# Performance work log

Hardware: AMD Instinct MI355X
Metric: run time of the kernel (lower is better)

The kernel has to match this reference:

```python
import jax, jax.numpy as jnp
import numpy as np

N = 20000   # nodes
E = 100000  # edges per relation
R = 4       # relations
H = 4       # heads
D = 64      # embed_dim (per-head dim == embed_dim in this module)
F = 128     # node_feat_dim
L = 2       # layers
EPS = 1e-5  # torch LayerNorm default


def setup_inputs() -> dict:
    key = jax.random.key(0)
    ks = jax.random.split(key, 32)
    s = 0.05
    inp = {}
    inp["nodes"] = jnp.arange(N)
    inp["node_features"] = jax.random.normal(ks[0], (N, F), jnp.float32)
    inp["betweenness"] = jax.random.uniform(ks[1], (N,), jnp.float32)
    inp["closeness"] = jax.random.uniform(ks[2], (N,), jnp.float32)
    inp["node_sign_influence"] = jax.random.normal(ks[3], (N,), jnp.float32)
    inp["edge_src"] = jax.random.randint(ks[4], (R, E), 0, N)
    inp["edge_tgt"] = jax.random.randint(ks[5], (R, E), 0, N)
    # encoder params
    inp["enc_Wf"] = jax.random.normal(ks[6], (F, D), jnp.float32) * s
    inp["enc_bf"] = jnp.full((D,), 0.01, jnp.float32)
    inp["enc_Wc"] = jax.random.normal(ks[7], (2, D), jnp.float32) * s
    inp["enc_bc"] = jnp.full((D,), 0.01, jnp.float32)
    # per-layer, per-relation attention params
    inp["Wq"] = jax.random.normal(ks[8], (L, R, D, D * H), jnp.float32) * s
    inp["bq"] = jnp.zeros((L, R, D * H), jnp.float32)
    inp["Wk"] = jax.random.normal(ks[9], (L, R, D, D * H), jnp.float32) * s
    inp["bk"] = jnp.zeros((L, R, D * H), jnp.float32)
    inp["Wv"] = jax.random.normal(ks[10], (L, R, D, D * H), jnp.float32) * s
    inp["bv"] = jnp.zeros((L, R, D * H), jnp.float32)
    inp["Wp"] = jax.random.normal(ks[11], (L, R * H * D, D), jnp.float32) * s
    inp["bp"] = jnp.zeros((L, D), jnp.float32)
    inp["sign_w"] = jax.random.normal(ks[12], (L, H, R), jnp.float32) * s
    inp["ln_g"] = jnp.ones((L, D), jnp.float32)
    inp["ln_b"] = jnp.zeros((L, D), jnp.float32)
    return inp


def reference(nodes, node_features, betweenness, closeness, node_sign_influence,
              edge_src, edge_tgt, enc_Wf, enc_bf, enc_Wc, enc_bc,
              Wq, bq, Wk, bk, Wv, bv, Wp, bp, sign_w, ln_g, ln_b):
    # CentralityAwareEncoder
    cen = jnp.stack([betweenness[nodes], closeness[nodes]], axis=1)  # [N, 2]
    x = node_features[nodes] @ enc_Wf + enc_bf + cen @ enc_Wc + enc_bc  # [N, D]
    n = x.shape[0]
    inv_sqrt_d = 1.0 / jnp.sqrt(jnp.float32(D))
    for l in range(L):  # structural loop over layers
        outs = []
        for r in range(R):  # structural loop over relations
            src, tgt = edge_src[r], edge_tgt[r]
            Q = (x @ Wq[l, r] + bq[l, r]).reshape(n, H, D)
            K = (x @ Wk[l, r] + bk[l, r]).reshape(n, H, D)
            V = (x @ Wv[l, r] + bv[l, r]).reshape(n, H, D)
            # edge-wise scores [E, H]
            scores = jnp.einsum('ehd,ehd->eh', Q[src], K[tgt]) * inv_sqrt_d
            scores = scores * (node_sign_influence[src][:, None] * sign_w[l, :, r][None, :])
            # segment softmax over src (all heads at once)
            mx = jax.ops.segment_max(scores, src, num_segments=n)
            ex = jnp.exp(scores - mx[src])
            den = jax.ops.segment_sum(ex, src, num_segments=n)
            attn = ex / (den[src] + 1e-10)  # [E, H]  (dropout: eval mode, identity)
            wV = V[tgt] * attn[..., None]   # [E, H, D]
            out = jax.ops.segment_sum(wV, src, num_segments=n)  # [N, H, D]
            outs.append(out.reshape(n, H * D))
        attn_out = jnp.concatenate(outs, axis=-1) @ Wp[l] + bp[l]  # [N, D]
        y = x + attn_out
        mu = y.mean(-1, keepdims=True)
        var = y.var(-1, keepdims=True)
        x = (y - mu) * jax.lax.rsqrt(var + EPS) * ln_g[l] + ln_b[l]
    return x
```

## Files before the change

### kernel.cpp

```cpp
#include <hip/hip_runtime.h>
#include <math.h>

#define NN 20000
#define EE 100000
#define RR 4
#define HH 4
#define DD 64
#define FF 128
#define LL 2

typedef __attribute__((ext_vector_type(8))) short bf16x8;
typedef __attribute__((ext_vector_type(4))) float f32x4;

__device__ __forceinline__ ushort f2bf(float f) {
  uint u = __float_as_uint(f);
  u += 0x7FFFu + ((u >> 16) & 1u);
  return (ushort)(u >> 16);
}
__device__ __forceinline__ float bf2f(ushort h) {
  return __uint_as_float((uint)h << 16);
}

__global__ __launch_bounds__(256) void enc_prep_kernel(
    const float* __restrict__ feat, const float* __restrict__ bet,
    const float* __restrict__ clo, const float* __restrict__ Wf,
    const float* __restrict__ bf, const float* __restrict__ Wc,
    const float* __restrict__ bc, float* __restrict__ x,
    ushort* __restrict__ xbf, const float* __restrict__ Wq,
    const float* __restrict__ bq, const float* __restrict__ Wk,
    const float* __restrict__ bk, const float* __restrict__ Wv,
    const float* __restrict__ bv, const float* __restrict__ Wp,
    ushort* __restrict__ mT, ushort* __restrict__ gT, float* __restrict__ cvec,
    float* __restrict__ gam) {
  const int t = threadIdx.x;
  if (blockIdx.x < 5000) {
    __shared__ float fs[4][FF];
    const int n0 = blockIdx.x * 4;
    for (int idx = t; idx < 4 * FF; idx += 256) {
      const int rr = idx >> 7, cc = idx & 127;
      const int n = n0 + rr;
      fs[rr][cc] = (n < NN) ? feat[(size_t)n * FF + cc] : 0.f;
    }
    __syncthreads();
    const int g = t >> 6, d = t & 63;
    const int n = n0 + g;
    if (n >= NN) return;
    float acc = bf[d] + bc[d] + bet[n] * Wc[d] + clo[n] * Wc[DD + d];
#pragma unroll 8
    for (int f = 0; f < FF; ++f) acc = fmaf(fs[g][f], Wf[f * DD + d], acc);
    x[(size_t)n * DD + d] = acc;
    xbf[(size_t)n * DD + d] = f2bf(acc);
    return;
  }
  const int idx = (blockIdx.x - 5000) * 256 + t;
  const int R1 = LL * RR * 272 * 64;
  const int R2 = LL * 64 * 1024;
  if (idx < R1) {
    const int lr = idx / (272 * 64);
    const int rem = idx % (272 * 64);
    const int col = rem >> 6, i = rem & 63;
    const float* wq = Wq + (size_t)lr * 64 * 256;
    const float* wk = Wk + (size_t)lr * 64 * 256;
    float v = 0.f;
    if (col < 256) {
      const int h = col >> 6, j = col & 63;
      const float* qa = wq + (size_t)i * 256 + h * 64;
      const float* kb = wk + (size_t)j * 256 + h * 64;
#pragma unroll 8
      for (int d = 0; d < 64; ++d) v = fmaf(qa[d], kb[d], v);
    } else if (col < 260) {
      const int h = col - 256;
      const float* qa = wq + (size_t)i * 256 + h * 64;
      const float* bb = bk + lr * 256 + h * 64;
#pragma unroll 8
      for (int d = 0; d < 64; ++d) v = fmaf(qa[d], bb[d], v);
    } else if (col < 264) {
      const int h = col - 260;
      const float* ka = wk + (size_t)i * 256 + h * 64;
      const float* bb = bq + lr * 256 + h * 64;
#pragma unroll 8
      for (int d = 0; d < 64; ++d) v = fmaf(ka[d], bb[d], v);
    }
    mT[idx] = f2bf(v);
  } else if (idx < R1 + R2) {
    const int id = idx - R1;
    const int lj = id >> 10;
    const int k = id & 1023;
    const int l = lj >> 6, j = lj & 63;
    const int r = k >> 8, h = (k >> 6) & 3, v_ = k & 63;
    const float* wv =
        Wv + (size_t)(l * RR + r) * 64 * 256 + (size_t)v_ * 256 + h * 64;
    const float* wp =
        Wp + (size_t)l * 65536 + (size_t)(r * 256 + h * 64) * 64 + j;
    float s = 0.f;
#pragma unroll 8
    for (int d = 0; d < 64; ++d) s = fmaf(wv[d], wp[d * 64], s);
    gT[id] = f2bf(s);
  } else if (idx < R1 + R2 + 512) {
    const int id = idx - R1 - R2;
    const int l = id >> 8, rj = id & 255;
    const int r = rj >> 6, j = rj & 63;
    const float* bb = bv + (l * RR + r) * 256;
    const float* wp = Wp + (size_t)l * 65536 + (size_t)(r * 256) * 64 + j;
    float s = 0.f;
    for (int q2 = 0; q2 < 256; ++q2) s = fmaf(bb[q2], wp[q2 * 64], s);
    cvec[id] = s;
  } else if (idx < R1 + R2 + 512 + 32) {
    const int id = idx - R1 - R2 - 512;
    const int lr = id >> 2, h = id & 3;
    const float* a = bq + lr * 256 + h * 64;
    const float* b2 = bk + lr * 256 + h * 64;
    float s = 0.f;
    for (int d = 0; d < 64; ++d) s = fmaf(a[d], b2[d], s);
    gam[id] = s;
  }
}

__global__ __launch_bounds__(256) void hist_kernel(
    const int* __restrict__ esrc, int* __restrict__ counts) {
  const int e = blockIdx.x * 256 + threadIdx.x;
  const int r = blockIdx.y;
  if (e < EE) atomicAdd(&counts[r * NN + esrc[(size_t)r * EE + e]], 1);
}

__global__ __launch_bounds__(1024) void scan_kernel(
    const int* __restrict__ counts, int* __restrict__ offs) {
  __shared__ int ts[1024];
  const int r = blockIdx.x, t = threadIdx.x;
  const int base = t * 20;
  int loc[20];
  int run = 0;
#pragma unroll
  for (int k = 0; k < 20; ++k) {
    const int i = base + k;
    const int v = (i < NN) ? counts[r * NN + i] : 0;
    run += v;
    loc[k] = run;
  }
  ts[t] = run;
  __syncthreads();
#pragma unroll
  for (int s = 1; s < 1024; s <<= 1) {
    const int add = (t >= s) ? ts[t - s] : 0;
    __syncthreads();
    ts[t] += add;
    __syncthreads();
  }
  const int prev = (t == 0) ? 0 : ts[t - 1];
#pragma unroll
  for (int k = 0; k < 20; ++k) {
    const int i = base + k;
    if (i < NN) offs[r * (NN + 1) + i + 1] = prev + loc[k];
  }
  if (t == 0) offs[r * (NN + 1)] = 0;
}

__global__ __launch_bounds__(256) void fill_kernel(
    const int* __restrict__ esrc, const int* __restrict__ etgt,
    const int* __restrict__ offs, int* __restrict__ cursor,
    int* __restrict__ csr) {
  const int e = blockIdx.x * 256 + threadIdx.x;
  const int r = blockIdx.y;
  if (e < EE) {
    const int s = esrc[(size_t)r * EE + e];
    const int pos = offs[r * (NN + 1) + s] + atomicAdd(&cursor[r * NN + s], 1);
    csr[(size_t)r * EE + pos] = etgt[(size_t)r * EE + e];
  }
}

__global__ __launch_bounds__(1024) void yattn_kernel(
    const ushort* __restrict__ xbf, const int* __restrict__ offs4,
    const int* __restrict__ csr4, const float* __restrict__ nsi,
    const float* __restrict__ sw_l, const float* __restrict__ gam_l,
    const ushort* __restrict__ mT_l, const ushort* __restrict__ gT,
    float* __restrict__ partial) {
  __shared__ ushort ys[16][264];
  __shared__ float alph[16][4];
  __shared__ float red[4][64][20];
  const int t = threadIdx.x;
  const int w = t >> 6, l = t & 63;
  const int hi = l >> 4, lo = l & 15;
  const int h = hi;
  const int m0 = blockIdx.x * 16;
  const int r = blockIdx.y;
  const ushort* mTr = mT_l + (size_t)r * 17408;

  const ushort* arow = xbf + (size_t)(m0 + lo) * 64 + hi * 8;
  const bf16x8 a0 = *(const bf16x8*)(arow);
  const bf16x8 a1 = *(const bf16x8*)(arow + 32);
  {
    const int col0 = w * 16;
    const ushort* brow = mTr + (size_t)(col0 + lo) * 64 + hi * 8;
    const bf16x8 b0 = *(const bf16x8*)(brow);
    const bf16x8 b1 = *(const bf16x8*)(brow + 32);
    f32x4 z = {0.f, 0.f, 0.f, 0.f};
    z = __builtin_amdgcn_mfma_f32_16x16x32_bf16(a0, b0, z, 0, 0, 0);
    z = __builtin_amdgcn_mfma_f32_16x16x32_bf16(a1, b1, z, 0, 0, 0);
    const int col = col0 + lo;
    const float wb = bf2f(mTr[(size_t)(260 + (col >> 6)) * 64 + (col & 63)]);
#pragma unroll
    for (int i = 0; i < 4; ++i) {
      ys[hi * 4 + i][col] = f2bf(z[i] + wb);
    }
  }
  if (w == 0) {
    const ushort* brow = mTr + (size_t)(256 + lo) * 64 + hi * 8;
    const bf16x8 b0 = *(const bf16x8*)(brow);
    const bf16x8 b1 = *(const bf16x8*)(brow + 32);
    f32x4 z = {0.f, 0.f, 0.f, 0.f};
    z = __builtin_amdgcn_mfma_f32_16x16x32_bf16(a0, b0, z, 0, 0, 0);
    z = __builtin_amdgcn_mfma_f32_16x16x32_bf16(a1, b1, z, 0, 0, 0);
    if (lo < 4) {
#pragma unroll
      for (int i = 0; i < 4; ++i) alph[hi * 4 + i][lo] = z[i];
    }
  }
  __syncthreads();

  {
    const int n = m0 + w;
    const int* offs = offs4 + r * (NN + 1);
    const int* csr = csr4 + (size_t)r * EE;
    const ushort4 yu = *(const ushort4*)&ys[w][l * 4];
    const float y0 = bf2f(yu.x), y1 = bf2f(yu.y), y2 = bf2f(yu.z),
                y3 = bf2f(yu.w);
    const float c2 = 0.18033688f * nsi[n] * sw_l[h * RR + r];
    const float ac2 = (alph[w][h] + gam_l[r * 4 + h]) * c2;
    const int s0 = offs[n], e0 = offs[n + 1];
    float denA = 0.f, oA0 = 0.f, oA1 = 0.f, oA2 = 0.f, oA3 = 0.f;
    float denB = 0.f, oB0 = 0.f, oB1 = 0.f, oB2 = 0.f, oB3 = 0.f;
    int i = s0;
    for (; i + 1 < e0; i += 2) {
      const int tgA = __builtin_amdgcn_readfirstlane(csr[i]);
      const int tgB = __builtin_amdgcn_readfirstlane(csr[i + 1]);
      const ushort4 cxA = *(const ushort4*)(xbf + (size_t)tgA * 64 + lo * 4);
      const ushort4 cxB = *(const ushort4*)(xbf + (size_t)tgB * 64 + lo * 4);
      const float xA0 = bf2f(cxA.x), xA1 = bf2f(cxA.y), xA2 = bf2f(cxA.z),
                  xA3 = bf2f(cxA.w);
      const float xB0 = bf2f(cxB.x), xB1 = bf2f(cxB.y), xB2 = bf2f(cxB.z),
                  xB3 = bf2f(cxB.w);
      float dA = y0 * xA0;
      float dB = y0 * xB0;
      dA = fmaf(y1, xA1, dA);
      dB = fmaf(y1, xB1, dB);
      dA = fmaf(y2, xA2, dA);
      dB = fmaf(y2, xB2, dB);
      dA = fmaf(y3, xA3, dA);
      dB = fmaf(y3, xB3, dB);
#pragma unroll
      for (int dd = 1; dd < 16; dd <<= 1) {
        dA += __shfl_xor(dA, dd);
        dB += __shfl_xor(dB, dd);
      }
      const float ewA = __builtin_amdgcn_exp2f(fmaf(dA, c2, ac2));
      const float ewB = __builtin_amdgcn_exp2f(fmaf(dB, c2, ac2));
      denA += ewA;
      denB += ewB;
      oA0 = fmaf(ewA, xA0, oA0);
      oB0 = fmaf(ewB, xB0, oB0);
      oA1 = fmaf(ewA, xA1, oA1);
      oB1 = fmaf(ewB, xB1, oB1);
      oA2 = fmaf(ewA, xA2, oA2);
      oB2 = fmaf(ewB, xB2, oB2);
      oA3 = fmaf(ewA, xA3, oA3);
      oB3 = fmaf(ewB, xB3, oB3);
    }
    if (i < e0) {
      const int tg = __builtin_amdgcn_readfirstlane(csr[i]);
      const ushort4 cx = *(const ushort4*)(xbf + (size_t)tg * 64 + lo * 4);
      const float x0 = bf2f(cx.x), x1 = bf2f(cx.y), x2 = bf2f(cx.z),
                  x3 = bf2f(cx.w);
      float d = y0 * x0;
      d = fmaf(y1, x1, d);
      d = fmaf(y2, x2, d);
      d = fmaf(y3, x3, d);
#pragma unroll
      for (int dd = 1; dd < 16; dd <<= 1) d += __shfl_xor(d, dd);
      const float ew = __builtin_amdgcn_exp2f(fmaf(d, c2, ac2));
      denA += ew;
      oA0 = fmaf(ew, x0, oA0);
      oA1 = fmaf(ew, x1, oA1);
      oA2 = fmaf(ew, x2, oA2);
      oA3 = fmaf(ew, x3, oA3);
    }
    const float inv = 1.f / (denA + denB + 1e-10f);
    ushort4 ou;
    ou.x = f2bf((oA0 + oB0) * inv);
    ou.y = f2bf((oA1 + oB1) * inv);
    ou.z = f2bf((oA2 + oB2) * inv);
    ou.w = f2bf((oA3 + oB3) * inv);
    *(ushort4*)&ys[w][l * 4] = ou;
  }
  __syncthreads();

  if (w < 4) {
    f32x4 acc[4] = {{0.f, 0.f, 0.f, 0.f},
                    {0.f, 0.f, 0.f, 0.f},
                    {0.f, 0.f, 0.f, 0.f},
                    {0.f, 0.f, 0.f, 0.f}};
#pragma unroll
    for (int ks = 0; ks < 2; ++ks) {
      const bf16x8 a = *(const bf16x8*)&ys[lo][w * 64 + ks * 32 + hi * 8];
#pragma unroll
      for (int nt = 0; nt < 4; ++nt) {
        const bf16x8 bb =
            *(const bf16x8*)(gT + (size_t)(nt * 16 + lo) * 1024 + r * 256 +
                             w * 64 + ks * 32 + hi * 8);
        acc[nt] =
            __builtin_amdgcn_mfma_f32_16x16x32_bf16(a, bb, acc[nt], 0, 0, 0);
      }
    }
#pragma unroll
    for (int nt = 0; nt < 4; ++nt) *(f32x4*)&red[w][l][nt * 4] = acc[nt];
  }
  __syncthreads();
  if (w == 0) {
    f32x4 fin[4];
#pragma unroll
    for (int nt = 0; nt < 4; ++nt) {
      f32x4 s = *(const f32x4*)&red[0][l][nt * 4];
      s += *(const f32x4*)&red[1][l][nt * 4];
      s += *(const f32x4*)&red[2][l][nt * 4];
      s += *(const f32x4*)&red[3][l][nt * 4];
      fin[nt] = s;
    }
#pragma unroll
    for (int i = 0; i < 4; ++i) {
      const int gr = m0 + hi * 4 + i;
#pragma unroll
      for (int nt = 0; nt < 4; ++nt) {
        partial[((size_t)r * NN + gr) * 64 + nt * 16 + lo] = fin[nt][i];
      }
    }
  }
}

__global__ __launch_bounds__(256) void ln_kernel(
    const float* __restrict__ partial, const float* __restrict__ xin,
    const float* __restrict__ bp, const float* __restrict__ g,
    const float* __restrict__ b, const int* __restrict__ offs4,
    const float* __restrict__ cvec_l, float* __restrict__ xout,
    ushort* __restrict__ xbf_out) {
  const int t = threadIdx.x;
  const int w = t >> 6, l = t & 63;
  const int m0 = blockIdx.x * 16;
#pragma unroll
  for (int k = 0; k < 4; ++k) {
    const int n = m0 + w * 4 + k;
    float v = partial[((size_t)0 * NN + n) * 64 + l] +
              partial[((size_t)1 * NN + n) * 64 + l] +
              partial[((size_t)2 * NN + n) * 64 + l] +
              partial[((size_t)3 * NN + n) * 64 + l];
#pragma unroll
    for (int r = 0; r < 4; ++r) {
      const bool nz = offs4[r * (NN + 1) + n + 1] > offs4[r * (NN + 1) + n];
      v += nz ? cvec_l[r * 64 + l] : 0.f;
    }
    const float y = v + bp[l] + xin[(size_t)n * 64 + l];
    float s = y, s2 = y * y;
#pragma unroll
    for (int dd = 1; dd < 64; dd <<= 1) {
      s += __shfl_xor(s, dd);
      s2 += __shfl_xor(s2, dd);
    }
    const float mu = s * (1.f / 64.f);
    const float var = s2 * (1.f / 64.f) - mu * mu;
    const float xo = (y - mu) * rsqrtf(var + 1e-5f) * g[l] + b[l];
    xout[(size_t)n * 64 + l] = xo;
    if (xbf_out) xbf_out[(size_t)n * 64 + l] = f2bf(xo);
  }
}

extern "C" void kernel_launch(void* const* d_in, const int* in_sizes, int n_in,
                              void* d_out, int out_size, void* d_ws,
                              size_t ws_size, hipStream_t stream) {
  const float* feat = (const float*)d_in[1];
  const float* bet = (const float*)d_in[2];
  const float* clo = (const float*)d_in[3];
  const float* nsi = (const float*)d_in[4];
  const int* esrc = (const int*)d_in[5];
  const int* etgt = (const int*)d_in[6];
  const float* Wf = (const float*)d_in[7];
  const float* bf = (const float*)d_in[8];
  const float* Wc = (const float*)d_in[9];
  const float* bc = (const float*)d_in[10];
  const float* Wq = (const float*)d_in[11];
  const float* bq = (const float*)d_in[12];
  const float* Wk = (const float*)d_in[13];
  const float* bk = (const float*)d_in[14];
  const float* Wv = (const float*)d_in[15];
  const float* bv = (const float*)d_in[16];
  const float* Wp = (const float*)d_in[17];
  const float* bp = (const float*)d_in[18];
  const float* sw = (const float*)d_in[19];
  const float* lng = (const float*)d_in[20];
  const float* lnb = (const float*)d_in[21];
  float* out = (float*)d_out;

  char* base = (char*)d_ws;
  size_t off = 0;
  auto alloc = [&](size_t bytes) {
    void* p = base + off;
    off += (bytes + 255) & ~(size_t)255;
    return p;
  };
  float* xa = (float*)alloc((size_t)NN * DD * 4);
  float* xb = (float*)alloc((size_t)NN * DD * 4);
  ushort* xbf = (ushort*)alloc((size_t)NN * DD * 2);
  float* partial = (float*)alloc((size_t)RR * NN * 64 * 4);
  ushort* mT = (ushort*)alloc((size_t)LL * RR * 272 * 64 * 2);
  ushort* gT = (ushort*)alloc((size_t)LL * 64 * 1024 * 2);
  float* cvec = (float*)alloc((size_t)LL * RR * 64 * 4);
  float* gam = (float*)alloc((size_t)LL * RR * HH * 4);
  int* counts = (int*)alloc((size_t)RR * NN * 4);
  int* offsb = (int*)alloc((size_t)RR * (NN + 1) * 4);
  int* csr = (int*)alloc((size_t)RR * EE * 4);
  (void)ws_size;

  hipMemsetAsync(counts, 0, (size_t)RR * NN * 4, stream);
  {
    dim3 gg((EE + 255) / 256, RR);
    hipLaunchKernelGGL(hist_kernel, gg, dim3(256), 0, stream, esrc, counts);
  }
  hipLaunchKernelGGL(scan_kernel, dim3(RR), dim3(1024), 0, stream, counts,
                     offsb);
  hipMemsetAsync(counts, 0, (size_t)RR * NN * 4, stream);
  {
    dim3 gg((EE + 255) / 256, RR);
    hipLaunchKernelGGL(fill_kernel, gg, dim3(256), 0, stream, esrc, etgt, offsb,
                       counts, csr);
  }

  hipLaunchKernelGGL(enc_prep_kernel, dim3(6059), dim3(256), 0, stream, feat,
                     bet, clo, Wf, bf, Wc, bc, xa, xbf, Wq, bq, Wk, bk, Wv, bv,
                     Wp, mT, gT, cvec, gam);

  for (int l = 0; l < LL; ++l) {
    const float* xin = (l == 0) ? xa : xb;
    float* xout = (l == LL - 1) ? out : xb;
    ushort* xbf_next = (l == LL - 1) ? (ushort*)nullptr : xbf;
    hipLaunchKernelGGL(yattn_kernel, dim3(NN / 16, RR), dim3(1024), 0, stream,
                       xbf, offsb, csr, nsi, sw + l * HH * RR, gam + l * 16,
                       mT + (size_t)l * RR * 17408, gT + (size_t)l * 65536,
                       partial);
    hipLaunchKernelGGL(ln_kernel, dim3(NN / 16), dim3(256), 0, stream, partial,
                       xin, bp + l * 64, lng + l * 64, lnb + l * 64, offsb,
                       cvec + l * 256, xout, xbf_next);
  }
}
```

Before: 329.8 us.

## Shrink attention blocks to 256 threads with per-wave multi-node loops

Cuts the yattn kernel block from 1024 to 256 threads. Each wave now computes four column tiles of the Y projection and handles four nodes' edge aggregation in sequence. The output projection is reorganised so each wave owns a 16-column slice over the full K=256, which removes the cross-wave LDS reduction, its shared buffer and one barrier. The aim is higher occupancy, less shared memory and fewer synchronisations. The cost is less parallelism per node and serialised edge loops within each wave.

```diff
diff --git a/kernel.cpp b/kernel.cpp
--- a/kernel.cpp
+++ b/kernel.cpp
@@ -168,7 +168,7 @@
   }
 }
 
-__global__ __launch_bounds__(1024) void yattn_kernel(
+__global__ __launch_bounds__(256) void yattn_kernel(
     const ushort* __restrict__ xbf, const int* __restrict__ offs4,
     const int* __restrict__ csr4, const float* __restrict__ nsi,
     const float* __restrict__ sw_l, const float* __restrict__ gam_l,
@@ -176,7 +176,6 @@
     float* __restrict__ partial) {
   __shared__ ushort ys[16][264];
   __shared__ float alph[16][4];
-  __shared__ float red[4][64][20];
   const int t = threadIdx.x;
   const int w = t >> 6, l = t & 63;
   const int hi = l >> 4, lo = l & 15;
@@ -188,8 +187,9 @@
   const ushort* arow = xbf + (size_t)(m0 + lo) * 64 + hi * 8;
   const bf16x8 a0 = *(const bf16x8*)(arow);
   const bf16x8 a1 = *(const bf16x8*)(arow + 32);
-  {
-    const int col0 = w * 16;
+#pragma unroll
+  for (int nt = 0; nt < 4; ++nt) {
+    const int col0 = w * 64 + nt * 16;
     const ushort* brow = mTr + (size_t)(col0 + lo) * 64 + hi * 8;
     const bf16x8 b0 = *(const bf16x8*)(brow);
     const bf16x8 b1 = *(const bf16x8*)(brow + 32);
@@ -203,7 +203,7 @@
       ys[hi * 4 + i][col] = f2bf(z[i] + wb);
     }
   }
-  if (w == 0) {
+  if (w == 3) {
     const ushort* brow = mTr + (size_t)(256 + lo) * 64 + hi * 8;
     const bf16x8 b0 = *(const bf16x8*)(brow);
     const bf16x8 b1 = *(const bf16x8*)(brow + 32);
@@ -217,15 +217,19 @@
   }
   __syncthreads();
 
-  {
-    const int n = m0 + w;
-    const int* offs = offs4 + r * (NN + 1);
-    const int* csr = csr4 + (size_t)r * EE;
-    const ushort4 yu = *(const ushort4*)&ys[w][l * 4];
+  const int* offs = offs4 + r * (NN + 1);
+  const int* csr = csr4 + (size_t)r * EE;
+  const float swh = sw_l[h * RR + r];
+  const float gamh = gam_l[r * 4 + h];
+#pragma unroll
+  for (int k = 0; k < 4; ++k) {
+    const int idx = w * 4 + k;
+    const int n = m0 + idx;
+    const ushort4 yu = *(const ushort4*)&ys[idx][l * 4];
     const float y0 = bf2f(yu.x), y1 = bf2f(yu.y), y2 = bf2f(yu.z),
                 y3 = bf2f(yu.w);
-    const float c2 = 0.18033688f * nsi[n] * sw_l[h * RR + r];
-    const float ac2 = (alph[w][h] + gam_l[r * 4 + h]) * c2;
+    const float c2 = 0.18033688f * nsi[n] * swh;
+    const float ac2 = (alph[idx][h] + gamh) * c2;
     const int s0 = offs[n], e0 = offs[n + 1];
     float denA = 0.f, oA0 = 0.f, oA1 = 0.f, oA2 = 0.f, oA3 = 0.f;
     float denB = 0.f, oB0 = 0.f, oB1 = 0.f, oB2 = 0.f, oB3 = 0.f;
@@ -289,49 +293,21 @@
     ou.y = f2bf((oA1 + oB1) * inv);
     ou.z = f2bf((oA2 + oB2) * inv);
     ou.w = f2bf((oA3 + oB3) * inv);
-    *(ushort4*)&ys[w][l * 4] = ou;
+    *(ushort4*)&ys[idx][l * 4] = ou;
   }
   __syncthreads();
 
-  if (w < 4) {
-    f32x4 acc[4] = {{0.f, 0.f, 0.f, 0.f},
-                    {0.f, 0.f, 0.f, 0.f},
-                    {0.f, 0.f, 0.f, 0.f},
-                    {0.f, 0.f, 0.f, 0.f}};
-#pragma unroll
-    for (int ks = 0; ks < 2; ++ks) {
-      const bf16x8 a = *(const bf16x8*)&ys[lo][w * 64 + ks * 32 + hi * 8];
-#pragma unroll
-      for (int nt = 0; nt < 4; ++nt) {
-        const bf16x8 bb =
-            *(const bf16x8*)(gT + (size_t)(nt * 16 + lo) * 1024 + r * 256 +
-                             w * 64 + ks * 32 + hi * 8);
-        acc[nt] =
-            __builtin_amdgcn_mfma_f32_16x16x32_bf16(a, bb, acc[nt], 0, 0, 0);
-      }
-    }
-#pragma unroll
-    for (int nt = 0; nt < 4; ++nt) *(f32x4*)&red[w][l][nt * 4] = acc[nt];
-  }
-  __syncthreads();
-  if (w == 0) {
-    f32x4 fin[4];
-#pragma unroll
-    for (int nt = 0; nt < 4; ++nt) {
-      f32x4 s = *(const f32x4*)&red[0][l][nt * 4];
-      s += *(const f32x4*)&red[1][l][nt * 4];
-      s += *(const f32x4*)&red[2][l][nt * 4];
-      s += *(const f32x4*)&red[3][l][nt * 4];
-      fin[nt] = s;
-    }
-#pragma unroll
-    for (int i = 0; i < 4; ++i) {
-      const int gr = m0 + hi * 4 + i;
-#pragma unroll
-      for (int nt = 0; nt < 4; ++nt) {
-        partial[((size_t)r * NN + gr) * 64 + nt * 16 + lo] = fin[nt][i];
-      }
-    }
+  f32x4 acc = {0.f, 0.f, 0.f, 0.f};
+#pragma unroll
+  for (int ks = 0; ks < 8; ++ks) {
+    const bf16x8 a = *(const bf16x8*)&ys[lo][ks * 32 + hi * 8];
+    const bf16x8 bb = *(const bf16x8*)(gT + (size_t)(w * 16 + lo) * 1024 +
+                                       r * 256 + ks * 32 + hi * 8);
+    acc = __builtin_amdgcn_mfma_f32_16x16x32_bf16(a, bb, acc, 0, 0, 0);
+  }
+#pragma unroll
+  for (int i = 0; i < 4; ++i) {
+    partial[((size_t)r * NN + m0 + hi * 4 + i) * 64 + w * 16 + lo] = acc[i];
   }
 }
 
@@ -439,7 +415,7 @@
     const float* xin = (l == 0) ? xa : xb;
     float* xout = (l == LL - 1) ? out : xb;
     ushort* xbf_next = (l == LL - 1) ? (ushort*)nullptr : xbf;
-    hipLaunchKernelGGL(yattn_kernel, dim3(NN / 16, RR), dim3(1024), 0, stream,
+    hipLaunchKernelGGL(yattn_kernel, dim3(NN / 16, RR), dim3(256), 0, stream,
                        xbf, offsb, csr, nsi, sw + l * HH * RR, gam + l * 16,
                        mT + (size_t)l * RR * 17408, gT + (size_t)l * 65536,
                        partial);
```

After: 278.6 us. 15.5% less time.
